# Kernel optimization log

Hardware: AMD Instinct MI355X
Metric: run time of the kernel (lower is better)

The kernel has to match this reference:

```python
import jax, jax.numpy as jnp
import numpy as np

B, S, D, H = 4, 2048, 512, 8
DH = D // H  # head dim = 64
NEG = -1000000.0


def setup_inputs() -> dict:
    key = jax.random.key(0)
    ks = jax.random.split(key, 13)
    s = 1.0 / np.sqrt(D)
    return {
        "Q": jax.random.normal(ks[0], (B, S, D), jnp.float32),
        "K": jax.random.normal(ks[1], (B, S, D), jnp.float32),
        "V": jax.random.normal(ks[2], (B, S, D), jnp.float32),
        "Wq": jax.random.normal(ks[3], (D, D), jnp.float32) * s,
        "bq": jnp.zeros((D,), jnp.float32),
        "Wk": jax.random.normal(ks[4], (D, D), jnp.float32) * s,
        "bk": jnp.zeros((D,), jnp.float32),
        "Wv": jax.random.normal(ks[5], (D, D), jnp.float32) * s,
        "bv": jnp.zeros((D,), jnp.float32),
        "Wo": jax.random.normal(ks[6], (D, D), jnp.float32) * s,
        "bo": jnp.zeros((D,), jnp.float32),
        "masked": jax.random.randint(ks[7], (B,), 1, S + 1, jnp.int64),
    }


def _heads(x):
    # [B,S,D] -> [B,H,S,DH]
    return x.reshape(B, S, H, DH).transpose(0, 2, 1, 3)


def reference(Q, K, V, Wq, bq, Wk, bk, Wv, bv, Wo, bo, masked):
    q = _heads(Q @ Wq.T + bq)
    k = _heads(K @ Wk.T + bk)
    v = _heads(V @ Wv.T + bv)
    scores = jnp.einsum("bhqd,bhkd->bhqk", q, k) / jnp.sqrt(jnp.asarray(DH, q.dtype))
    # valid-length key mask, per batch (same for every head and query row)
    key_mask = jnp.arange(S)[None, None, None, :] < masked[:, None, None, None]
    scores = jnp.where(key_mask, scores, jnp.asarray(NEG, scores.dtype))
    weights = jax.nn.softmax(scores, axis=-1)
    out = jnp.einsum("bhqk,bhkd->bhqd", weights, v)  # [B,H,S,DH]
    out = out.transpose(0, 2, 1, 3).reshape(B, S, D)
    return out @ Wo.T + bo
```

## Files before the change

kernel.cpp:

```cpp
#include <hip/hip_runtime.h>


typedef __attribute__((ext_vector_type(8))) short short8;
typedef __attribute__((ext_vector_type(4))) short short4v;
typedef __attribute__((ext_vector_type(4))) float f32x4;

#define MFMA16(a, b, c) __builtin_amdgcn_mfma_f32_16x16x32_bf16(a, b, c, 0, 0, 0)

#define SCALE_LOG2 0.18033688011112042f
#define FIXED_M    32.0f
#define MASKED_E2  -200.0f

__device__ __forceinline__ unsigned short f2bf(float f) {
    unsigned int x = __float_as_uint(f);
    unsigned int r = (x + 0x7fffu + ((x >> 16) & 1u)) >> 16;
    return (unsigned short)r;
}
__device__ __forceinline__ short8 load8(const unsigned short* p) {
    return *reinterpret_cast<const short8*>(p);
}
__device__ __forceinline__ short8 pack8(const float* f) {
    const float4 a = *reinterpret_cast<const float4*>(f);
    const float4 b = *reinterpret_cast<const float4*>(f + 4);
    short8 r;
    r[0] = (short)f2bf(a.x); r[1] = (short)f2bf(a.y);
    r[2] = (short)f2bf(a.z); r[3] = (short)f2bf(a.w);
    r[4] = (short)f2bf(b.x); r[5] = (short)f2bf(b.y);
    r[6] = (short)f2bf(b.z); r[7] = (short)f2bf(b.w);
    return r;
}

__global__ __launch_bounds__(256)
void gemm128(const void* __restrict__ A0, const void* __restrict__ A1,
             const void* __restrict__ A2,
             const float* __restrict__ W0, const float* __restrict__ W1,
             const float* __restrict__ W2,
             const float* __restrict__ b0, const float* __restrict__ b1,
             const float* __restrict__ b2,
             void* __restrict__ o0, void* __restrict__ o1,
             void* __restrict__ o2,
             int out_mode, int a_f32)
{
    __shared__ unsigned short As[128][40];
    __shared__ unsigned short Bs[128][40];

    const int z = blockIdx.y;
    const void*  A    = (z == 0) ? A0 : (z == 1) ? A1 : A2;
    const float* W    = (z == 0) ? W0 : (z == 1) ? W1 : W2;
    const float* bias = (z == 0) ? b0 : (z == 1) ? b1 : b2;
    void*        out  = (z == 0) ? o0 : (z == 1) ? o1 : o2;

    const int f    = blockIdx.x;
    const int xcd  = f & 7;
    const int slot = f >> 3;
    const int col0 = (slot & 3) * 128;
    const int row0 = ((slot >> 2) * 8 + xcd) * 128;

    const int tid  = threadIdx.x;
    const int lane = tid & 63;
    const int w    = tid >> 6;
    const int quad = lane >> 4;
    const int nlow = lane & 15;
    const int wm   = w >> 1;
    const int wn   = w & 1;

    const int srow = tid >> 1;
    const int skc  = (tid & 1) * 16;

    f32x4 acc[4][4];
#pragma unroll
    for (int fi = 0; fi < 4; fi++)
#pragma unroll
        for (int g = 0; g < 4; g++) acc[fi][g] = (f32x4){0.f, 0.f, 0.f, 0.f};

    for (int k0 = 0; k0 < 512; k0 += 32) {
        const long aoff = (long)(row0 + srow) * 512 + k0 + skc;
        if (a_f32) {
            const float* pa = (const float*)A + aoff;
            *reinterpret_cast<short8*>(&As[srow][skc])     = pack8(pa);
            *reinterpret_cast<short8*>(&As[srow][skc + 8]) = pack8(pa + 8);
        } else {
            const unsigned short* pa = (const unsigned short*)A + aoff;
            *reinterpret_cast<short8*>(&As[srow][skc])     = load8(pa);
            *reinterpret_cast<short8*>(&As[srow][skc + 8]) = load8(pa + 8);
        }
        const float* pb = W + (long)(col0 + srow) * 512 + k0 + skc;
        *reinterpret_cast<short8*>(&Bs[srow][skc])     = pack8(pb);
        *reinterpret_cast<short8*>(&Bs[srow][skc + 8]) = pack8(pb + 8);
        __syncthreads();

        short8 af[4], bf[4];
#pragma unroll
        for (int fi = 0; fi < 4; fi++)
            af[fi] = load8(&As[wm * 64 + fi * 16 + nlow][quad * 8]);
#pragma unroll
        for (int g = 0; g < 4; g++)
            bf[g] = load8(&Bs[wn * 64 + g * 16 + nlow][quad * 8]);
#pragma unroll
        for (int fi = 0; fi < 4; fi++)
#pragma unroll
            for (int g = 0; g < 4; g++)
                acc[fi][g] = MFMA16(af[fi], bf[g], acc[fi][g]);
        __syncthreads();
    }

#pragma unroll
    for (int g = 0; g < 4; g++) {
        const int j = col0 + wn * 64 + g * 16 + nlow;
        const float bj = bias[j];
#pragma unroll
        for (int fi = 0; fi < 4; fi++) {
#pragma unroll
            for (int r = 0; r < 4; r++) {
                const int i = row0 + wm * 64 + fi * 16 + quad * 4 + r;
                const float v = acc[fi][g][r] + bj;
                if (out_mode == 0) {
                    const int b = i >> 11, s = i & 2047;
                    const int h = j >> 6, dh = j & 63;
                    ((unsigned short*)out)[(((b * 8 + h) * 2048) + s) * 64 + dh] = f2bf(v);
                } else {
                    ((float*)out)[(long)i * 512 + j] = v;
                }
            }
        }
    }
}

__global__ __launch_bounds__(256)
void attn_kernel(const unsigned short* __restrict__ qp,
                 const unsigned short* __restrict__ kp,
                 const unsigned short* __restrict__ vp,
                 const void* __restrict__ masked,
                 unsigned short* __restrict__ out)
{
    __shared__ unsigned short Ks[32][72];
    __shared__ unsigned short Vt[64][40];
    __shared__ unsigned short Ps[4][16][44];

    const int tid  = threadIdx.x;
    const int lane = tid & 63;
    const int w    = tid >> 6;
    const int quad = lane >> 4;
    const int nlow = lane & 15;

    const int b  = blockIdx.z;
    const int h  = blockIdx.y;
    const int q0 = blockIdx.x * 64 + w * 16;
    const long base = ((long)(b * 8 + h)) * 2048 * 64;

    const long long first = *reinterpret_cast<const long long*>(masked);
    int kmax;
    if ((first >> 32) != 0) kmax = reinterpret_cast<const int*>(masked)[b];
    else                    kmax = (int)reinterpret_cast<const long long*>(masked)[b];
    kmax = min(max(kmax, 1), 2048);

    const unsigned short* qrow = qp + base + (long)(q0 + nlow) * 64;
    const short8 aq0 = load8(qrow + quad * 8);
    const short8 aq1 = load8(qrow + 32 + quad * 8);

    short8 ones;
#pragma unroll
    for (int j = 0; j < 8; j++) ones[j] = (short)0x3F80;

    f32x4 o_acc[4], lacc;
#pragma unroll
    for (int vb = 0; vb < 4; vb++) o_acc[vb] = (f32x4){0.f, 0.f, 0.f, 0.f};
    lacc = (f32x4){0.f, 0.f, 0.f, 0.f};

    const int srow = tid >> 3;
    const int skk  = (tid & 7) * 8;
    const int kg   = srow >> 3;
    const int ko   = srow & 7;
    const int nkt  = (kmax + 31) >> 5;

    for (int kt = 0; kt < nkt; kt++) {
        const int k0 = kt * 32;
        *reinterpret_cast<short8*>(&Ks[srow][skk]) =
            load8(&kp[base + (long)(k0 + srow) * 64 + skk]);
        short8 vv = load8(&vp[base + (long)(k0 + srow) * 64 + skk]);
#pragma unroll
        for (int j = 0; j < 8; j++) {
            const int dh = skk + j;
            Vt[dh][((kg ^ ((dh >> 3) & 3)) << 3) + ko] = (unsigned short)vv[j];
        }
        __syncthreads();

        f32x4 sacc[2];
        sacc[0] = (f32x4){0.f, 0.f, 0.f, 0.f};
        sacc[1] = (f32x4){0.f, 0.f, 0.f, 0.f};
#pragma unroll
        for (int kb = 0; kb < 2; kb++) {
            short8 bk0 = load8(&Ks[kb * 16 + nlow][quad * 8]);
            short8 bk1 = load8(&Ks[kb * 16 + nlow][32 + quad * 8]);
            sacc[kb] = MFMA16(aq0, bk0, sacc[kb]);
            sacc[kb] = MFMA16(aq1, bk1, sacc[kb]);
        }

#pragma unroll
        for (int kb = 0; kb < 2; kb++) {
            const bool valid = (k0 + kb * 16 + nlow) < kmax;
#pragma unroll
            for (int r = 0; r < 4; r++) {
                const float e = valid ? fmaf(sacc[kb][r], SCALE_LOG2, -FIXED_M)
                                      : MASKED_E2;
                Ps[w][quad * 4 + r][kb * 16 + nlow] = f2bf(exp2f(e));
            }
        }

        __threadfence_block();

        const short4v apl = *reinterpret_cast<const short4v*>(&Ps[w][nlow][quad * 8]);
        const short4v aph = *reinterpret_cast<const short4v*>(&Ps[w][nlow][quad * 8 + 4]);
        short8 ap;
        ap[0] = apl[0]; ap[1] = apl[1]; ap[2] = apl[2]; ap[3] = apl[3];
        ap[4] = aph[0]; ap[5] = aph[1]; ap[6] = aph[2]; ap[7] = aph[3];

        lacc = MFMA16(ap, ones, lacc);
#pragma unroll
        for (int vb = 0; vb < 4; vb++) {
            const int dhr = vb * 16 + nlow;
            short8 bv = load8(&Vt[dhr][(quad ^ ((dhr >> 3) & 3)) << 3]);
            o_acc[vb] = MFMA16(ap, bv, o_acc[vb]);
        }
        __syncthreads();
    }

    float inv_l[4];
#pragma unroll
    for (int r = 0; r < 4; r++) inv_l[r] = 1.0f / lacc[r];
#pragma unroll
    for (int vb = 0; vb < 4; vb++) {
#pragma unroll
        for (int r = 0; r < 4; r++) {
            const int s   = q0 + quad * 4 + r;
            const int col = h * 64 + vb * 16 + nlow;
            out[(long)(b * 2048 + s) * 512 + col] = f2bf(o_acc[vb][r] * inv_l[r]);
        }
    }
}

extern "C" void kernel_launch(void* const* d_in, const int* in_sizes, int n_in,
                              void* d_out, int out_size, void* d_ws, size_t ws_size,
                              hipStream_t stream)
{
    const void*  Q  = d_in[0];
    const void*  K  = d_in[1];
    const void*  V  = d_in[2];
    const float* Wq = (const float*)d_in[3];
    const float* bq = (const float*)d_in[4];
    const float* Wk = (const float*)d_in[5];
    const float* bk = (const float*)d_in[6];
    const float* Wv = (const float*)d_in[7];
    const float* bv = (const float*)d_in[8];
    const float* Wo = (const float*)d_in[9];
    const float* bo = (const float*)d_in[10];
    const void*  masked = d_in[11];

    unsigned short* qp = (unsigned short*)d_ws;
    unsigned short* kp = qp + 8192 * 512;
    unsigned short* vp = kp + 8192 * 512;
    unsigned short* ao = vp + 8192 * 512;

    gemm128<<<dim3(256, 3), 256, 0, stream>>>(
        Q, K, V, Wq, Wk, Wv, bq, bk, bv, qp, kp, vp, 0, 1);
    attn_kernel<<<dim3(32, 8, 4), 256, 0, stream>>>(qp, kp, vp, masked, ao);
    gemm128<<<dim3(256, 1), 256, 0, stream>>>(
        ao, ao, ao, Wo, Wo, Wo, bo, bo, bo, d_out, d_out, d_out, 1, 0);
}
```

Before: 214.4 us.

## Pre-convert inputs to bf16 and use direct global-to-LDS loads in GEMM

Adds a separate kernel that converts Q, K, V and all weight matrices from fp32 to bf16 into workspace. The projection GEMMs then read bf16 directly through global_load_lds (asynchronous direct-to-LDS copies) into an XOR-swizzled LDS layout, with the K tile widened from 32 to 64. This removes the per-tile fp32 unpack and convert work and the register staging from the GEMM inner loop. The cost is an extra kernel launch and a full extra read and write pass over the inputs, and the conversion is still redone on every call.

New measurement: 178.7 us. 16.7% less time.

```diff
diff --git a/kernel.cpp b/kernel.cpp
--- a/kernel.cpp
+++ b/kernel.cpp
@@ -1,9 +1,11 @@
 #include <hip/hip_runtime.h>
+#include <stdint.h>
 
 
 typedef __attribute__((ext_vector_type(8))) short short8;
 typedef __attribute__((ext_vector_type(4))) short short4v;
 typedef __attribute__((ext_vector_type(4))) float f32x4;
+typedef __attribute__((ext_vector_type(4))) unsigned short u16x4;
 
 #define MFMA16(a, b, c) __builtin_amdgcn_mfma_f32_16x16x32_bf16(a, b, c, 0, 0, 0)
 
@@ -19,36 +21,51 @@
 __device__ __forceinline__ short8 load8(const unsigned short* p) {
     return *reinterpret_cast<const short8*>(p);
 }
-__device__ __forceinline__ short8 pack8(const float* f) {
-    const float4 a = *reinterpret_cast<const float4*>(f);
-    const float4 b = *reinterpret_cast<const float4*>(f + 4);
-    short8 r;
-    r[0] = (short)f2bf(a.x); r[1] = (short)f2bf(a.y);
-    r[2] = (short)f2bf(a.z); r[3] = (short)f2bf(a.w);
-    r[4] = (short)f2bf(b.x); r[5] = (short)f2bf(b.y);
-    r[6] = (short)f2bf(b.z); r[7] = (short)f2bf(b.w);
-    return r;
+__device__ __forceinline__ void gload_lds16(const unsigned short* g, unsigned short* l) {
+    __builtin_amdgcn_global_load_lds(
+        (const __attribute__((address_space(1))) unsigned int*)g,
+        (__attribute__((address_space(3))) unsigned int*)l, 16, 0, 0);
 }
 
 __global__ __launch_bounds__(256)
-void gemm128(const void* __restrict__ A0, const void* __restrict__ A1,
-             const void* __restrict__ A2,
-             const float* __restrict__ W0, const float* __restrict__ W1,
-             const float* __restrict__ W2,
+void convert_bf16(const float4* __restrict__ Q, const float4* __restrict__ K,
+                  const float4* __restrict__ V, const float4* __restrict__ Wq,
+                  const float4* __restrict__ Wk, const float4* __restrict__ Wv,
+                  const float4* __restrict__ Wo, u16x4* __restrict__ dst)
+{
+    const int n = 3407872;
+    for (int i = blockIdx.x * 256 + threadIdx.x; i < n; i += gridDim.x * 256) {
+        const float4* src; int off;
+        if      (i < 1048576) { src = Q;  off = i; }
+        else if (i < 2097152) { src = K;  off = i - 1048576; }
+        else if (i < 3145728) { src = V;  off = i - 2097152; }
+        else if (i < 3211264) { src = Wq; off = i - 3145728; }
+        else if (i < 3276800) { src = Wk; off = i - 3211264; }
+        else if (i < 3342336) { src = Wv; off = i - 3276800; }
+        else                  { src = Wo; off = i - 3342336; }
+        const float4 v = src[off];
+        u16x4 r;
+        r[0] = f2bf(v.x); r[1] = f2bf(v.y); r[2] = f2bf(v.z); r[3] = f2bf(v.w);
+        dst[i] = r;
+    }
+}
+
+__global__ __launch_bounds__(256)
+void gemm_bf(const unsigned short* __restrict__ Aall,
+             const unsigned short* __restrict__ Wall,
              const float* __restrict__ b0, const float* __restrict__ b1,
              const float* __restrict__ b2,
-             void* __restrict__ o0, void* __restrict__ o1,
-             void* __restrict__ o2,
-             int out_mode, int a_f32)
-{
-    __shared__ unsigned short As[128][40];
-    __shared__ unsigned short Bs[128][40];
+             void* __restrict__ outall, int out_mode)
+{
+    __shared__ unsigned short As[128 * 64];
+    __shared__ unsigned short Bs[128 * 64];
 
     const int z = blockIdx.y;
-    const void*  A    = (z == 0) ? A0 : (z == 1) ? A1 : A2;
-    const float* W    = (z == 0) ? W0 : (z == 1) ? W1 : W2;
+    const unsigned short* A = Aall + (long)z * 4194304;
+    const unsigned short* W = Wall + z * 262144;
     const float* bias = (z == 0) ? b0 : (z == 1) ? b1 : b2;
-    void*        out  = (z == 0) ? o0 : (z == 1) ? o1 : o2;
+    void* out = (out_mode == 0)
+        ? (void*)((unsigned short*)outall + (long)z * 4194304) : outall;
 
     const int f    = blockIdx.x;
     const int xcd  = f & 7;
@@ -61,46 +78,56 @@
     const int w    = tid >> 6;
     const int quad = lane >> 4;
     const int nlow = lane & 15;
-    const int wm   = w >> 1;
-    const int wn   = w & 1;
-
-    const int srow = tid >> 1;
-    const int skc  = (tid & 1) * 16;
+    const int wm   = w >> 1, wn = w & 1;
+
+    const unsigned short* ag[4];
+    const unsigned short* wg[4];
+    unsigned short *la[4], *lb[4];
+#pragma unroll
+    for (int i = 0; i < 4; i++) {
+        const int s = i * 256 + tid;
+        const int r = s >> 3, kcl = s & 7;
+        const int kg = kcl ^ (r & 7);
+        ag[i] = A + (long)(row0 + r) * 512 + kg * 8;
+        wg[i] = W + (long)(col0 + r) * 512 + kg * 8;
+        const int ldso = i * 2048 + ((tid >> 6) << 9);
+        la[i] = As + ldso;
+        lb[i] = Bs + ldso;
+    }
 
     f32x4 acc[4][4];
 #pragma unroll
-    for (int fi = 0; fi < 4; fi++)
-#pragma unroll
-        for (int g = 0; g < 4; g++) acc[fi][g] = (f32x4){0.f, 0.f, 0.f, 0.f};
-
-    for (int k0 = 0; k0 < 512; k0 += 32) {
-        const long aoff = (long)(row0 + srow) * 512 + k0 + skc;
-        if (a_f32) {
-            const float* pa = (const float*)A + aoff;
-            *reinterpret_cast<short8*>(&As[srow][skc])     = pack8(pa);
-            *reinterpret_cast<short8*>(&As[srow][skc + 8]) = pack8(pa + 8);
-        } else {
-            const unsigned short* pa = (const unsigned short*)A + aoff;
-            *reinterpret_cast<short8*>(&As[srow][skc])     = load8(pa);
-            *reinterpret_cast<short8*>(&As[srow][skc + 8]) = load8(pa + 8);
-        }
-        const float* pb = W + (long)(col0 + srow) * 512 + k0 + skc;
-        *reinterpret_cast<short8*>(&Bs[srow][skc])     = pack8(pb);
-        *reinterpret_cast<short8*>(&Bs[srow][skc + 8]) = pack8(pb + 8);
-        __syncthreads();
-
-        short8 af[4], bf[4];
-#pragma unroll
-        for (int fi = 0; fi < 4; fi++)
-            af[fi] = load8(&As[wm * 64 + fi * 16 + nlow][quad * 8]);
-#pragma unroll
-        for (int g = 0; g < 4; g++)
-            bf[g] = load8(&Bs[wn * 64 + g * 16 + nlow][quad * 8]);
-#pragma unroll
-        for (int fi = 0; fi < 4; fi++)
-#pragma unroll
-            for (int g = 0; g < 4; g++)
-                acc[fi][g] = MFMA16(af[fi], bf[g], acc[fi][g]);
+    for (int t = 0; t < 4; t++)
+#pragma unroll
+        for (int g = 0; g < 4; g++) acc[t][g] = (f32x4){0.f, 0.f, 0.f, 0.f};
+
+    for (int k0 = 0; k0 < 512; k0 += 64) {
+#pragma unroll
+        for (int i = 0; i < 4; i++) {
+            gload_lds16(ag[i] + k0, la[i]);
+            gload_lds16(wg[i] + k0, lb[i]);
+        }
+        __syncthreads();
+
+        short8 af[4][2], bf[4][2];
+#pragma unroll
+        for (int t = 0; t < 4; t++) {
+            const int rowa = wm * 64 + t * 16 + nlow;
+            const int rowb = wn * 64 + t * 16 + nlow;
+#pragma unroll
+            for (int kc = 0; kc < 2; kc++) {
+                const int c = (kc * 4 + quad) ^ (nlow & 7);
+                af[t][kc] = load8(&As[(rowa * 8 + c) * 8]);
+                bf[t][kc] = load8(&Bs[(rowb * 8 + c) * 8]);
+            }
+        }
+#pragma unroll
+        for (int kc = 0; kc < 2; kc++)
+#pragma unroll
+            for (int t = 0; t < 4; t++)
+#pragma unroll
+                for (int g = 0; g < 4; g++)
+                    acc[t][g] = MFMA16(af[t][kc], bf[g][kc], acc[t][g]);
         __syncthreads();
     }
 
@@ -109,11 +136,11 @@
         const int j = col0 + wn * 64 + g * 16 + nlow;
         const float bj = bias[j];
 #pragma unroll
-        for (int fi = 0; fi < 4; fi++) {
+        for (int t = 0; t < 4; t++) {
 #pragma unroll
             for (int r = 0; r < 4; r++) {
-                const int i = row0 + wm * 64 + fi * 16 + quad * 4 + r;
-                const float v = acc[fi][g][r] + bj;
+                const int i = row0 + wm * 64 + t * 16 + quad * 4 + r;
+                const float v = acc[t][g][r] + bj;
                 if (out_mode == 0) {
                     const int b = i >> 11, s = i & 2047;
                     const int h = j >> 6, dh = j & 63;
@@ -206,7 +233,6 @@
                 Ps[w][quad * 4 + r][kb * 16 + nlow] = f2bf(exp2f(e));
             }
         }
-
         __threadfence_block();
 
         const short4v apl = *reinterpret_cast<const short4v*>(&Ps[w][nlow][quad * 8]);
@@ -243,27 +269,30 @@
                               void* d_out, int out_size, void* d_ws, size_t ws_size,
                               hipStream_t stream)
 {
-    const void*  Q  = d_in[0];
-    const void*  K  = d_in[1];
-    const void*  V  = d_in[2];
-    const float* Wq = (const float*)d_in[3];
-    const float* bq = (const float*)d_in[4];
-    const float* Wk = (const float*)d_in[5];
-    const float* bk = (const float*)d_in[6];
-    const float* Wv = (const float*)d_in[7];
-    const float* bv = (const float*)d_in[8];
-    const float* Wo = (const float*)d_in[9];
-    const float* bo = (const float*)d_in[10];
-    const void*  masked = d_in[11];
-
-    unsigned short* qp = (unsigned short*)d_ws;
-    unsigned short* kp = qp + 8192 * 512;
-    unsigned short* vp = kp + 8192 * 512;
-    unsigned short* ao = vp + 8192 * 512;
-
-    gemm128<<<dim3(256, 3), 256, 0, stream>>>(
-        Q, K, V, Wq, Wk, Wv, bq, bk, bv, qp, kp, vp, 0, 1);
+    const float4* Q  = (const float4*)d_in[0];
+    const float4* K  = (const float4*)d_in[1];
+    const float4* V  = (const float4*)d_in[2];
+    const float4* Wq = (const float4*)d_in[3];
+    const float*  bq = (const float*)d_in[4];
+    const float4* Wk = (const float4*)d_in[5];
+    const float*  bk = (const float*)d_in[6];
+    const float4* Wv = (const float4*)d_in[7];
+    const float*  bv = (const float*)d_in[8];
+    const float4* Wo = (const float4*)d_in[9];
+    const float*  bo = (const float*)d_in[10];
+    const void*   masked = d_in[11];
+
+    unsigned short* ws16 = (unsigned short*)d_ws;
+    unsigned short* QKVb = ws16;
+    unsigned short* Wb   = ws16 + 12582912;
+    unsigned short* qp   = ws16 + 13631488;
+    unsigned short* kp   = qp + 4194304;
+    unsigned short* vp   = kp + 4194304;
+    unsigned short* ao   = ws16;
+
+    convert_bf16<<<2048, 256, 0, stream>>>(Q, K, V, Wq, Wk, Wv, Wo, (u16x4*)ws16);
+    gemm_bf<<<dim3(256, 3), 256, 0, stream>>>(QKVb, Wb, bq, bk, bv, qp, 0);
     attn_kernel<<<dim3(32, 8, 4), 256, 0, stream>>>(qp, kp, vp, masked, ao);
-    gemm128<<<dim3(256, 1), 256, 0, stream>>>(
-        ao, ao, ao, Wo, Wo, Wo, bo, bo, bo, d_out, d_out, d_out, 1, 0);
-}
+    gemm_bf<<<dim3(256, 1), 256, 0, stream>>>(ao, Wb + 3 * 262144, bo, bo, bo,
+                                              d_out, 1);
+}
```
